# Optimization experiments

Measured on AMD Instinct MI355X. Metric: run time of the kernel, lower is better.

The kernel has to match this reference:

```python
import jax, jax.numpy as jnp
import numpy as np

N_FILTER, S_SUB, D_IN, K_STEP, TAO = 8, 5, 64, 3, 0.05
B, N = 100000, 100000


def setup_inputs() -> dict:
    key = jax.random.key(0)
    k1, k2, k3, k4, k5 = jax.random.split(key, 5)
    adjs = jax.random.uniform(k1, (B, S_SUB, S_SUB), jnp.float32)
    feature = jax.random.normal(k2, (N, D_IN), jnp.float32)
    idxs = jax.random.randint(k3, (B, S_SUB), 0, N)  # indexes into feature; row N is the zero pad row
    adjs_hidden = jax.random.uniform(k4, (N_FILTER, S_SUB * (S_SUB - 1) // 2), jnp.float32, minval=-1.0, maxval=1.0)
    features_hidden = jax.random.uniform(k5, (N_FILTER, S_SUB, D_IN), jnp.float32, minval=-1.0, maxval=1.0)
    return dict(adjs=adjs, feature=feature, idxs=idxs, adjs_hidden=adjs_hidden, features_hidden=features_hidden)


def _greedy_mask(total):
    # total: [B, F, m, s]. Greedy row-by-row argmax matching, columns consumed once.
    B_, F_, m, s = total.shape
    taken0 = jnp.zeros((B_, F_, s), bool).at[:, :, 0].set(True)  # column 0 reserved for row 0

    def step(taken, row_scores):  # row_scores: [B, F, s]
        scores = jnp.where(taken, jnp.asarray(-1.0, total.dtype), row_scores)
        idx = jnp.argmax(scores, axis=-1)  # [B, F]
        oh = jax.nn.one_hot(idx, s, dtype=total.dtype)
        return jnp.logical_or(taken, oh > 0), oh

    xs = jnp.moveaxis(total[:, :, 1:, :], 2, 0)  # [m-1, B, F, s]
    _, rows = jax.lax.scan(step, taken0, xs)  # rows: [m-1, B, F, s]
    row0 = jnp.zeros((B_, F_, s), total.dtype).at[:, :, 0].set(1.0)
    mask = jnp.concatenate([row0[None], rows], axis=0)  # [m, B, F, s]
    return jnp.moveaxis(mask, 0, 2)  # [B, F, m, s]


def reference(adjs, feature, idxs, adjs_hidden, features_hidden):
    F_, s, d = features_hidden.shape
    # symmetric hidden adjacency from sigmoid of upper-triangular params
    sig = jax.nn.sigmoid(adjs_hidden)
    iu0, iu1 = np.triu_indices(s, 1)
    A_h = (jnp.zeros((F_, s, s), adjs_hidden.dtype)
           .at[:, iu0, iu1].set(sig)
           .at[:, iu1, iu0].set(sig))
    # pad features with a zero row, gather subgraph node features
    feat = jnp.concatenate([feature, jnp.zeros((1, feature.shape[1]), feature.dtype)], axis=0)
    f = feat[idxs]  # [B, m, d]
    fh = features_hidden  # [F, s, d]

    total = jnp.zeros((f.shape[0], F_, f.shape[1], s), f.dtype)
    for hop in range(K_STEP):
        if hop != 0:
            f = jnp.einsum('bij,bjd->bid', adjs, f)
            fh = jnp.einsum('fij,fjd->fid', A_h, fh)
        sq_f = jnp.sum(f * f, axis=-1)    # [B, m]
        sq_h = jnp.sum(fh * fh, axis=-1)  # [F, s]
        cross = jnp.einsum('bme,fse->bfms', f, fh)  # [B, F, m, s]
        dist = sq_f[:, None, :, None] + sq_h[None, :, None, :] - 2.0 * cross
        total = total + jnp.exp(-dist / d / TAO)

    mask = _greedy_mask(total)
    return jnp.sum(total * mask, axis=(2, 3))  # [B, F]
```

## Files before the change

kernel.cpp:

```cpp
#include <hip/hip_runtime.h>
#include <math.h>

#define NF 8
#define SS 5
#define DIN 64
#define KSTEP 3
#define BT 32
#define FH_PAD 68
#define FSTR (SS*FH_PAD)
#define HOPSTR (NF*FSTR)

#define CS 0.45084219902780109f
#define CC 0.90168439805560218f

__device__ __forceinline__ float fexp2(float x) {
#if __has_builtin(__builtin_amdgcn_exp2f)
  return __builtin_amdgcn_exp2f(x);
#else
  return exp2f(x);
#endif
}


__global__ __launch_bounds__(256) void hidden_prep(
    const float* __restrict__ adjs_hidden,
    const float* __restrict__ features_hidden,
    float* __restrict__ ws)
{
  __shared__ float Ah[NF][SS][SS];
  __shared__ float buf[2][NF][SS][DIN];
  const int t = threadIdx.x;

  if (t < NF*SS*SS) ((float*)Ah)[t] = 0.0f;
  for (int i = t; i < NF*SS*DIN; i += 256) ((float*)buf[0])[i] = features_hidden[i];
  __syncthreads();
  if (t < NF*10) {
    const int iu0[10] = {0,0,0,0,1,1,1,2,2,3};
    const int iu1[10] = {1,2,3,4,2,3,4,3,4,4};
    int f = t / 10, k = t % 10;
    float sg = 1.0f / (1.0f + expf(-adjs_hidden[t]));
    Ah[f][iu0[k]][iu1[k]] = sg;
    Ah[f][iu1[k]][iu0[k]] = sg;
  }
  __syncthreads();

  int cur = 0;
  for (int h = 0; h < KSTEP; ++h) {
    for (int i = t; i < NF*SS*DIN; i += 256) {
      int f = i / (SS*DIN), s = (i / DIN) % SS, d = i % DIN;
      ws[h*HOPSTR + f*FSTR + s*FH_PAD + d] = buf[cur][f][s][d];
    }
    if (t < NF*SS) {
      float acc = 0.0f;
      int f = t / SS, s = t % SS;
      for (int d = 0; d < DIN; ++d) { float v = buf[cur][f][s][d]; acc = fmaf(v, v, acc); }
      ws[KSTEP*HOPSTR + h*NF*SS + t] = -acc * CS;
    }
    if (h + 1 < KSTEP) {
      __syncthreads();
      for (int i = t; i < NF*SS*DIN; i += 256) {
        int f = i / (SS*DIN), s = (i / DIN) % SS, d = i % DIN;
        float acc = 0.0f;
        for (int j = 0; j < SS; ++j) acc = fmaf(Ah[f][s][j], buf[cur][f][j][d], acc);
        buf[cur^1][f][s][d] = acc;
      }
      __syncthreads();
      cur ^= 1;
    }
  }
}

__global__ __launch_bounds__(256, 2) void kc_main(
    const float* __restrict__ adjs,
    const float* __restrict__ feature,
    const int* __restrict__ idxs,
    const float* __restrict__ ws,
    float* __restrict__ out,
    int B, int N)
{
  __shared__ float fh[KSTEP*HOPSTR];
  __shared__ float nsqh[KSTEP][NF][SS];
  __shared__ float fS[BT][SS][FH_PAD];
  __shared__ float adjS[BT][SS*SS];
  __shared__ float sqfS[BT][SS];
  __shared__ int   idxS[BT*SS];

  const int t = threadIdx.x;
  const int b0 = blockIdx.x * BT;

  for (int i = t; i < KSTEP*HOPSTR; i += 256) fh[i] = ws[i];
  for (int i = t; i < KSTEP*NF*SS; i += 256) ((float*)nsqh)[i] = ws[KSTEP*HOPSTR + i];
  for (int i = t; i < BT*SS*SS; i += 256) {
    int b = i / (SS*SS);
    ((float*)adjS)[i] = (b0 + b < B) ? adjs[(size_t)b0*SS*SS + i] : 0.0f;
  }
  for (int i = t; i < BT*SS; i += 256) {
    int b = i / SS;
    idxS[i] = (b0 + b < B) ? idxs[(size_t)b0*SS + i] : -1;
  }
  __syncthreads();

  for (int i = t; i < BT*SS*16; i += 256) {
    int row = i >> 4, d4 = i & 15;
    int id = idxS[row];
    float4 v = make_float4(0.f, 0.f, 0.f, 0.f);
    if ((unsigned)id < (unsigned)N)
      v = reinterpret_cast<const float4*>(feature)[(size_t)id*16 + d4];
    int b = row / SS, m = row % SS;
    *reinterpret_cast<float4*>(&fS[b][m][d4*4]) = v;
  }
  __syncthreads();

  const int b_i = t >> 3;
  const int f_  = t & 7;

  float total[SS][SS];
  #pragma unroll
  for (int m = 0; m < SS; ++m)
    #pragma unroll
    for (int s = 0; s < SS; ++s) total[m][s] = 0.0f;

  for (int hop = 0; hop < KSTEP; ++hop) {
    if (hop) {
      const int dbase = f_ * 8;
      float fo[SS][8];
      #pragma unroll
      for (int j = 0; j < SS; ++j)
        #pragma unroll
        for (int dd = 0; dd < 8; ++dd) fo[j][dd] = fS[b_i][j][dbase + dd];
      float fn[SS][8];
      #pragma unroll
      for (int m = 0; m < SS; ++m) {
        #pragma unroll
        for (int dd = 0; dd < 8; ++dd) fn[m][dd] = 0.0f;
        #pragma unroll
        for (int j = 0; j < SS; ++j) {
          float a = adjS[b_i][m*SS + j];
          #pragma unroll
          for (int dd = 0; dd < 8; ++dd) fn[m][dd] = fmaf(a, fo[j][dd], fn[m][dd]);
        }
      }
      __syncthreads();
      #pragma unroll
      for (int m = 0; m < SS; ++m)
        #pragma unroll
        for (int dd = 0; dd < 8; ++dd) fS[b_i][m][dbase + dd] = fn[m][dd];
      __syncthreads();
    }

    if (f_ < SS) {
      float acc = 0.0f;
      const float* fr = &fS[b_i][f_][0];
      #pragma unroll
      for (int d4 = 0; d4 < 16; ++d4) {
        float4 v = *reinterpret_cast<const float4*>(&fr[d4*4]);
        acc = fmaf(v.x, v.x, acc);
        acc = fmaf(v.y, v.y, acc);
        acc = fmaf(v.z, v.z, acc);
        acc = fmaf(v.w, v.w, acc);
      }
      sqfS[b_i][f_] = acc * CS;
    }
    __syncthreads();

    float cr[SS][SS];
    #pragma unroll
    for (int m = 0; m < SS; ++m)
      #pragma unroll
      for (int s = 0; s < SS; ++s) cr[m][s] = 0.0f;

    const float* fhh = &fh[hop*HOPSTR + f_*FSTR];
    #pragma unroll
    for (int d4 = 0; d4 < 16; ++d4) {
      float4 fv[SS], hv[SS];
      #pragma unroll
      for (int m = 0; m < SS; ++m)
        fv[m] = *reinterpret_cast<const float4*>(&fS[b_i][m][d4*4]);
      #pragma unroll
      for (int s = 0; s < SS; ++s)
        hv[s] = *reinterpret_cast<const float4*>(&fhh[s*FH_PAD + d4*4]);
      #pragma unroll
      for (int m = 0; m < SS; ++m)
        #pragma unroll
        for (int s = 0; s < SS; ++s) {
          cr[m][s] = fmaf(fv[m].x, hv[s].x, cr[m][s]);
          cr[m][s] = fmaf(fv[m].y, hv[s].y, cr[m][s]);
          cr[m][s] = fmaf(fv[m].z, hv[s].z, cr[m][s]);
          cr[m][s] = fmaf(fv[m].w, hv[s].w, cr[m][s]);
        }
    }

    float sqf2[SS], nh[SS];
    #pragma unroll
    for (int m = 0; m < SS; ++m) sqf2[m] = sqfS[b_i][m];
    #pragma unroll
    for (int s = 0; s < SS; ++s) nh[s] = nsqh[hop][f_][s];
    #pragma unroll
    for (int m = 0; m < SS; ++m)
      #pragma unroll
      for (int s = 0; s < SS; ++s) {
        float arg = fmaf(CC, cr[m][s], nh[s] - sqf2[m]);
        total[m][s] += fexp2(arg);
      }
  }

  float res = total[0][0];
  int taken = 1;
  #pragma unroll
  for (int r = 1; r < SS; ++r) {
    float best = -2.0f; int bi = 0;
    #pragma unroll
    for (int s = 0; s < SS; ++s) {
      float sc = ((taken >> s) & 1) ? -1.0f : total[r][s];
      if (sc > best) { best = sc; bi = s; }
    }
    res += best;
    taken |= (1 << bi);
  }
  const int bg = b0 + b_i;
  if (bg < B) out[(size_t)bg*NF + f_] = res;
}

extern "C" void kernel_launch(void* const* d_in, const int* in_sizes, int n_in,
                              void* d_out, int out_size, void* d_ws, size_t ws_size,
                              hipStream_t stream) {
  const float* adjs            = (const float*)d_in[0];
  const float* feature         = (const float*)d_in[1];
  const int*   idxs            = (const int*)d_in[2];
  const float* adjs_hidden     = (const float*)d_in[3];
  const float* features_hidden = (const float*)d_in[4];
  float* out = (float*)d_out;
  float* ws  = (float*)d_ws;

  const int B = in_sizes[0] / (SS*SS);
  const int N = in_sizes[1] / DIN;

  hipLaunchKernelGGL(hidden_prep, dim3(1), dim3(256), 0, stream,
                     adjs_hidden, features_hidden, ws);
  const int nblk = (B + BT - 1) / BT;
  hipLaunchKernelGGL(kc_main, dim3(nblk), dim3(256), 0, stream,
                     adjs, feature, idxs, ws, out, B, N);
}
```

Baseline: 151.1 us.

## Read hidden features from global cache and drop block-wide LDS staging and barriers

Stops copying the full multi-hop hidden feature table and its norms into shared memory in every block. These are now read directly from the workspace in global memory, and a cleaner unpadded layout is written by the prep kernel. Each 8-thread group now gathers its own batch item's indices, adjacency and feature rows. All __syncthreads are removed, which relies on the 8 threads of a batch item sharing one wavefront. The much smaller LDS footprint should allow higher occupancy and removes the per-block preload traffic, at the cost of repeated global/L1 reads of the hidden features inside the inner loop.

After: 375.3 us. 2.48x slower.

```diff
diff --git a/kernel.cpp b/kernel.cpp
--- a/kernel.cpp
+++ b/kernel.cpp
@@ -7,8 +7,9 @@
 #define KSTEP 3
 #define BT 32
 #define FH_PAD 68
-#define FSTR (SS*FH_PAD)
-#define HOPSTR (NF*FSTR)
+#define FH_STR (SS*DIN)
+#define HOPSTR (NF*FH_STR)
+#define NS_OFF (KSTEP*HOPSTR)
 
 #define CS 0.45084219902780109f
 #define CC 0.90168439805560218f
@@ -20,7 +21,6 @@
   return exp2f(x);
 #endif
 }
-
 
 __global__ __launch_bounds__(256) void hidden_prep(
     const float* __restrict__ adjs_hidden,
@@ -46,15 +46,13 @@
 
   int cur = 0;
   for (int h = 0; h < KSTEP; ++h) {
-    for (int i = t; i < NF*SS*DIN; i += 256) {
-      int f = i / (SS*DIN), s = (i / DIN) % SS, d = i % DIN;
-      ws[h*HOPSTR + f*FSTR + s*FH_PAD + d] = buf[cur][f][s][d];
-    }
+    for (int i = t; i < NF*SS*DIN; i += 256)
+      ws[h*HOPSTR + i] = ((float*)buf[cur])[i];
     if (t < NF*SS) {
       float acc = 0.0f;
       int f = t / SS, s = t % SS;
       for (int d = 0; d < DIN; ++d) { float v = buf[cur][f][s][d]; acc = fmaf(v, v, acc); }
-      ws[KSTEP*HOPSTR + h*NF*SS + t] = -acc * CS;
+      ws[NS_OFF + h*NF*SS + t] = -acc * CS;
     }
     if (h + 1 < KSTEP) {
       __syncthreads();
@@ -70,7 +68,7 @@
   }
 }
 
-__global__ __launch_bounds__(256, 2) void kc_main(
+__global__ __launch_bounds__(256) void kc_main(
     const float* __restrict__ adjs,
     const float* __restrict__ feature,
     const int* __restrict__ idxs,
@@ -78,41 +76,34 @@
     float* __restrict__ out,
     int B, int N)
 {
-  __shared__ float fh[KSTEP*HOPSTR];
-  __shared__ float nsqh[KSTEP][NF][SS];
   __shared__ float fS[BT][SS][FH_PAD];
-  __shared__ float adjS[BT][SS*SS];
-  __shared__ float sqfS[BT][SS];
-  __shared__ int   idxS[BT*SS];
-
-  const int t = threadIdx.x;
-  const int b0 = blockIdx.x * BT;
-
-  for (int i = t; i < KSTEP*HOPSTR; i += 256) fh[i] = ws[i];
-  for (int i = t; i < KSTEP*NF*SS; i += 256) ((float*)nsqh)[i] = ws[KSTEP*HOPSTR + i];
-  for (int i = t; i < BT*SS*SS; i += 256) {
-    int b = i / (SS*SS);
-    ((float*)adjS)[i] = (b0 + b < B) ? adjs[(size_t)b0*SS*SS + i] : 0.0f;
-  }
-  for (int i = t; i < BT*SS; i += 256) {
-    int b = i / SS;
-    idxS[i] = (b0 + b < B) ? idxs[(size_t)b0*SS + i] : -1;
-  }
-  __syncthreads();
-
-  for (int i = t; i < BT*SS*16; i += 256) {
-    int row = i >> 4, d4 = i & 15;
-    int id = idxS[row];
-    float4 v = make_float4(0.f, 0.f, 0.f, 0.f);
-    if ((unsigned)id < (unsigned)N)
-      v = reinterpret_cast<const float4*>(feature)[(size_t)id*16 + d4];
-    int b = row / SS, m = row % SS;
-    *reinterpret_cast<float4*>(&fS[b][m][d4*4]) = v;
-  }
-  __syncthreads();
-
+  __shared__ float adjS[BT][28];
+  __shared__ float sqfS[BT][8];
+
+  const int t   = threadIdx.x;
   const int b_i = t >> 3;
   const int f_  = t & 7;
+  const int bg  = blockIdx.x * BT + b_i;
+  const bool valid = bg < B;
+
+  #pragma unroll
+  for (int k = f_; k < SS*SS; k += 8)
+    adjS[b_i][k] = valid ? adjs[(size_t)bg*(SS*SS) + k] : 0.0f;
+
+  int idxv[SS];
+  #pragma unroll
+  for (int m = 0; m < SS; ++m)
+    idxv[m] = valid ? idxs[bg*SS + m] : -1;
+  #pragma unroll
+  for (int m = 0; m < SS; ++m) {
+    #pragma unroll
+    for (int h2 = 0; h2 < 2; ++h2) {
+      float4 v = make_float4(0.f, 0.f, 0.f, 0.f);
+      if ((unsigned)idxv[m] < (unsigned)N)
+        v = reinterpret_cast<const float4*>(feature)[(size_t)idxv[m]*16 + f_*2 + h2];
+      *reinterpret_cast<float4*>(&fS[b_i][m][f_*8 + h2*4]) = v;
+    }
+  }
 
   float total[SS][SS];
   #pragma unroll
@@ -120,32 +111,38 @@
     #pragma unroll
     for (int s = 0; s < SS; ++s) total[m][s] = 0.0f;
 
+  #pragma unroll 1
   for (int hop = 0; hop < KSTEP; ++hop) {
     if (hop) {
       const int dbase = f_ * 8;
+      float a[SS][SS];
+      #pragma unroll
+      for (int m = 0; m < SS; ++m)
+        #pragma unroll
+        for (int j = 0; j < SS; ++j) a[m][j] = adjS[b_i][m*SS + j];
       float fo[SS][8];
       #pragma unroll
       for (int j = 0; j < SS; ++j)
         #pragma unroll
-        for (int dd = 0; dd < 8; ++dd) fo[j][dd] = fS[b_i][j][dbase + dd];
-      float fn[SS][8];
+        for (int h2 = 0; h2 < 2; ++h2) {
+          float4 v = *reinterpret_cast<const float4*>(&fS[b_i][j][dbase + h2*4]);
+          fo[j][h2*4+0] = v.x; fo[j][h2*4+1] = v.y; fo[j][h2*4+2] = v.z; fo[j][h2*4+3] = v.w;
+        }
       #pragma unroll
       for (int m = 0; m < SS; ++m) {
-        #pragma unroll
-        for (int dd = 0; dd < 8; ++dd) fn[m][dd] = 0.0f;
-        #pragma unroll
-        for (int j = 0; j < SS; ++j) {
-          float a = adjS[b_i][m*SS + j];
+        float fn[8];
+        #pragma unroll
+        for (int dd = 0; dd < 8; ++dd) fn[dd] = 0.0f;
+        #pragma unroll
+        for (int j = 0; j < SS; ++j)
           #pragma unroll
-          for (int dd = 0; dd < 8; ++dd) fn[m][dd] = fmaf(a, fo[j][dd], fn[m][dd]);
+          for (int dd = 0; dd < 8; ++dd) fn[dd] = fmaf(a[m][j], fo[j][dd], fn[dd]);
+        #pragma unroll
+        for (int h2 = 0; h2 < 2; ++h2) {
+          float4 v = make_float4(fn[h2*4+0], fn[h2*4+1], fn[h2*4+2], fn[h2*4+3]);
+          *reinterpret_cast<float4*>(&fS[b_i][m][dbase + h2*4]) = v;
         }
       }
-      __syncthreads();
-      #pragma unroll
-      for (int m = 0; m < SS; ++m)
-        #pragma unroll
-        for (int dd = 0; dd < 8; ++dd) fS[b_i][m][dbase + dd] = fn[m][dd];
-      __syncthreads();
     }
 
     if (f_ < SS) {
@@ -161,7 +158,6 @@
       }
       sqfS[b_i][f_] = acc * CS;
     }
-    __syncthreads();
 
     float cr[SS][SS];
     #pragma unroll
@@ -169,7 +165,7 @@
       #pragma unroll
       for (int s = 0; s < SS; ++s) cr[m][s] = 0.0f;
 
-    const float* fhh = &fh[hop*HOPSTR + f_*FSTR];
+    const float4* hv4 = reinterpret_cast<const float4*>(ws + hop*HOPSTR + f_*FH_STR);
     #pragma unroll
     for (int d4 = 0; d4 < 16; ++d4) {
       float4 fv[SS], hv[SS];
@@ -178,7 +174,7 @@
         fv[m] = *reinterpret_cast<const float4*>(&fS[b_i][m][d4*4]);
       #pragma unroll
       for (int s = 0; s < SS; ++s)
-        hv[s] = *reinterpret_cast<const float4*>(&fhh[s*FH_PAD + d4*4]);
+        hv[s] = hv4[s*16 + d4];
       #pragma unroll
       for (int m = 0; m < SS; ++m)
         #pragma unroll
@@ -193,8 +189,9 @@
     float sqf2[SS], nh[SS];
     #pragma unroll
     for (int m = 0; m < SS; ++m) sqf2[m] = sqfS[b_i][m];
-    #pragma unroll
-    for (int s = 0; s < SS; ++s) nh[s] = nsqh[hop][f_][s];
+    const float* nsq = ws + NS_OFF + hop*NF*SS + f_*SS;
+    #pragma unroll
+    for (int s = 0; s < SS; ++s) nh[s] = nsq[s];
     #pragma unroll
     for (int m = 0; m < SS; ++m)
       #pragma unroll
@@ -217,8 +214,7 @@
     res += best;
     taken |= (1 << bi);
   }
-  const int bg = b0 + b_i;
-  if (bg < B) out[(size_t)bg*NF + f_] = res;
+  if (valid) out[(size_t)bg*NF + f_] = res;
 }
 
 extern "C" void kernel_launch(void* const* d_in, const int* in_sizes, int n_in,
```
